# Optimization experiments

Hardware: AMD Instinct MI355X
Metric: run time of the kernel (lower is better)

## Reference

```python
import jax, jax.numpy as jnp
import numpy as np

FLOOR = 1e-06


def _ema(x, w):
    # x: [B, C, T], w: [C] clamped to [0, 1]
    w = jnp.clip(w, 0.0, 1.0)
    xt = jnp.moveaxis(x, 2, 0)  # [T, B, C]
    init = x[:, :, 0]           # [B, C]

    def step(acc, xi):
        acc = w * xi + (1.0 - w) * acc
        return acc, acc

    _, ys = jax.lax.scan(step, init, xt)  # ys: [T, B, C]
    return jnp.moveaxis(ys, 0, 2)         # [B, C, T]


def setup_inputs() -> dict:
    key = jax.random.key(0)
    k1, = jax.random.split(key, 1)
    B, C, T = 128, 64, 8000
    x = jax.random.uniform(k1, (B, C, T), dtype=jnp.float32)
    alpha = jnp.full((C,), 0.96, dtype=jnp.float32)
    delta = jnp.full((C,), 2.0, dtype=jnp.float32)
    root = jnp.full((C,), 2.0, dtype=jnp.float32)
    ema_weights = jnp.full((C,), 0.04, dtype=jnp.float32)
    return {"x": x, "alpha": alpha, "delta": delta, "root": root,
            "ema_weights": ema_weights}


def reference(x, alpha, delta, root, ema_weights):
    alpha = jnp.minimum(alpha, 1.0)          # [C]
    root = jnp.maximum(root, 1.0)            # [C]
    ema = _ema(x, ema_weights)               # [B, C, T]
    one_over_root = 1.0 / root
    a = alpha[None, :, None]
    d = delta[None, :, None]
    r = one_over_root[None, :, None]
    out = (x / (FLOOR + ema) ** a + d) ** r - d ** r
    return out
```

## Files before the change

kernel.cpp:

```cpp
#include <hip/hip_runtime.h>
#include <math.h>

#define T_LEN   8000
#define NT4     (T_LEN / 256)
#define TAILOFF (NT4 * 256)
#define FLOORV  1e-6f

__device__ __forceinline__ float pcen_pt(float xv, float em,
                                         float na, float d, float r, float dr)
{
    float u  = __builtin_amdgcn_exp2f(na * __builtin_amdgcn_logf(FLOORV + em));
    float b2 = fmaf(xv, u, d);
    return __builtin_amdgcn_exp2f(r * __builtin_amdgcn_logf(b2)) - dr;
}

__global__ __launch_bounds__(256, 8) void pcen_kernel(
    const float* __restrict__ x,
    const float* __restrict__ alpha,
    const float* __restrict__ delta,
    const float* __restrict__ root,
    const float* __restrict__ emaw,
    float* __restrict__ out,
    int C, int rows)
{
    const int wave = threadIdx.x >> 6;
    const int lane = threadIdx.x & 63;
    const int row  = blockIdx.x * 4 + wave;
    if (row >= rows) return;
    const int c = row % C;

    const float a  = fminf(alpha[c], 1.0f);
    const float d  = delta[c];
    const float rt = fmaxf(root[c], 1.0f);
    const float r  = 1.0f / rt;
    const float w  = fminf(fmaxf(emaw[c], 0.0f), 1.0f);
    const float q  = 1.0f - w;
    const float na = -a;
    const float dr = __builtin_amdgcn_exp2f(r * __builtin_amdgcn_logf(d));
    const float q2 = q * q, q4 = q2 * q2;

    const float*  xr  = x   + (size_t)row * T_LEN;
    float*        orw = out + (size_t)row * T_LEN;
    const float4* xv4 = (const float4*)xr;
    float4*       ov4 = (float4*)orw;

    float e = xr[0];

    float4 v = xv4[lane];
    for (int t = 0; t < NT4; ++t) {
        float4 cur = v;
        if (t + 1 < NT4) v = xv4[(t + 1) * 64 + lane];

        float A = w * cur.x;
        A = fmaf(q, A, w * cur.y);
        A = fmaf(q, A, w * cur.z);
        A = fmaf(q, A, w * cur.w);
        float D = q4;

        #pragma unroll
        for (int off = 1; off < 64; off <<= 1) {
            float Alo = __shfl_up(A, off);
            float Dlo = __shfl_up(D, off);
            if (lane >= off) { A = fmaf(D, Alo, A); D *= Dlo; }
        }

        float Aex = __shfl_up(A, 1);
        float Dex = __shfl_up(D, 1);
        float ein = (lane == 0) ? e : fmaf(Dex, e, Aex);

        float A63 = __shfl(A, 63);
        float D63 = __shfl(D, 63);
        float enext = fmaf(D63, e, A63);

        float e0 = fmaf(q, ein, w * cur.x);
        float e1 = fmaf(q, e0,  w * cur.y);
        float e2 = fmaf(q, e1,  w * cur.z);
        float e3 = fmaf(q, e2,  w * cur.w);
        float4 o;
        o.x = pcen_pt(cur.x, e0, na, d, r, dr);
        o.y = pcen_pt(cur.y, e1, na, d, r, dr);
        o.z = pcen_pt(cur.z, e2, na, d, r, dr);
        o.w = pcen_pt(cur.w, e3, na, d, r, dr);
        ov4[t * 64 + lane] = o;

        e = enext;
    }

    {
        float xt = xr[TAILOFF + lane];
        float A = w * xt;
        float D = q;
        #pragma unroll
        for (int off = 1; off < 64; off <<= 1) {
            float Alo = __shfl_up(A, off);
            float Dlo = __shfl_up(D, off);
            if (lane >= off) { A = fmaf(D, Alo, A); D *= Dlo; }
        }
        float em = fmaf(D, e, A);
        orw[TAILOFF + lane] = pcen_pt(xt, em, na, d, r, dr);
    }
}

extern "C" void kernel_launch(void* const* d_in, const int* in_sizes, int n_in,
                              void* d_out, int out_size, void* d_ws, size_t ws_size,
                              hipStream_t stream) {
    const float* x     = (const float*)d_in[0];
    const float* alpha = (const float*)d_in[1];
    const float* delta = (const float*)d_in[2];
    const float* root  = (const float*)d_in[3];
    const float* emaw  = (const float*)d_in[4];
    float* out = (float*)d_out;

    const int C    = in_sizes[1];
    const int rows = in_sizes[0] / T_LEN;

    const int blocks = (rows + 3) / 4;
    pcen_kernel<<<blocks, 256, 0, stream>>>(x, alpha, delta, root, emaw, out, C, rows);
}
```

Before: 451.6 us.

## Precompute decay powers for wave scan and deepen load prefetch to two tiles

The wave-level scan no longer carries and shuffles a decay factor D. Because the decay is a uniform power of q, the per-step multipliers q^(4*2^k), the per-lane prefix power and q^256 are computed once before the loop, which roughly halves the shuffles and multiplies per scan step. The tail scan gets the same treatment with powers of q. The x load is also prefetched two iterations ahead instead of one, costing an extra float4 of registers and a redundant reload of the last tile at the end.

```diff
diff --git a/kernel.cpp b/kernel.cpp
--- a/kernel.cpp
+++ b/kernel.cpp
@@ -37,7 +37,18 @@
     const float q  = 1.0f - w;
     const float na = -a;
     const float dr = __builtin_amdgcn_exp2f(r * __builtin_amdgcn_logf(d));
+
     const float q2 = q * q, q4 = q2 * q2;
+    const float c0 = q4, c1 = c0 * c0, c2 = c1 * c1,
+                c3 = c2 * c2, c4 = c3 * c3, c5 = c4 * c4;
+    const float q256 = c5 * c5;
+    float qpow = 1.0f;
+    qpow *= (lane & 1 ) ? c0 : 1.0f;
+    qpow *= (lane & 2 ) ? c1 : 1.0f;
+    qpow *= (lane & 4 ) ? c2 : 1.0f;
+    qpow *= (lane & 8 ) ? c3 : 1.0f;
+    qpow *= (lane & 16) ? c4 : 1.0f;
+    qpow *= (lane & 32) ? c5 : 1.0f;
 
     const float*  xr  = x   + (size_t)row * T_LEN;
     float*        orw = out + (size_t)row * T_LEN;
@@ -46,31 +57,33 @@
 
     float e = xr[0];
 
-    float4 v = xv4[lane];
+    float4 va = xv4[lane];
+    float4 vb = xv4[64 + lane];
+
     for (int t = 0; t < NT4; ++t) {
-        float4 cur = v;
-        if (t + 1 < NT4) v = xv4[(t + 1) * 64 + lane];
+        float4 cur = va;
+        va = vb;
+        const int pf = (t + 2 < NT4) ? (t + 2) : (NT4 - 1);
+        vb = xv4[pf * 64 + lane];
 
         float A = w * cur.x;
         A = fmaf(q, A, w * cur.y);
         A = fmaf(q, A, w * cur.z);
         A = fmaf(q, A, w * cur.w);
-        float D = q4;
 
-        #pragma unroll
-        for (int off = 1; off < 64; off <<= 1) {
-            float Alo = __shfl_up(A, off);
-            float Dlo = __shfl_up(D, off);
-            if (lane >= off) { A = fmaf(D, Alo, A); D *= Dlo; }
-        }
+        float s0 = __shfl_up(A, 1);  if (lane >= 1 ) A = fmaf(c0, s0, A);
+        float s1 = __shfl_up(A, 2);  if (lane >= 2 ) A = fmaf(c1, s1, A);
+        float s2 = __shfl_up(A, 4);  if (lane >= 4 ) A = fmaf(c2, s2, A);
+        float s3 = __shfl_up(A, 8);  if (lane >= 8 ) A = fmaf(c3, s3, A);
+        float s4 = __shfl_up(A, 16); if (lane >= 16) A = fmaf(c4, s4, A);
+        float s5 = __shfl_up(A, 32); if (lane >= 32) A = fmaf(c5, s5, A);
 
         float Aex = __shfl_up(A, 1);
-        float Dex = __shfl_up(D, 1);
-        float ein = (lane == 0) ? e : fmaf(Dex, e, Aex);
+        Aex = (lane == 0) ? 0.0f : Aex;
+        float ein = fmaf(qpow, e, Aex);
 
         float A63 = __shfl(A, 63);
-        float D63 = __shfl(D, 63);
-        float enext = fmaf(D63, e, A63);
+        float enext = fmaf(q256, e, A63);
 
         float e0 = fmaf(q, ein, w * cur.x);
         float e1 = fmaf(q, e0,  w * cur.y);
@@ -88,15 +101,23 @@
 
     {
         float xt = xr[TAILOFF + lane];
-        float A = w * xt;
-        float D = q;
-        #pragma unroll
-        for (int off = 1; off < 64; off <<= 1) {
-            float Alo = __shfl_up(A, off);
-            float Dlo = __shfl_up(D, off);
-            if (lane >= off) { A = fmaf(D, Alo, A); D *= Dlo; }
-        }
-        float em = fmaf(D, e, A);
+        float A  = w * xt;
+        const float d0 = q, d1 = d0 * d0, d2 = d1 * d1,
+                    d3 = d2 * d2, d4 = d3 * d3, d5 = d4 * d4;
+        float s0 = __shfl_up(A, 1);  if (lane >= 1 ) A = fmaf(d0, s0, A);
+        float s1 = __shfl_up(A, 2);  if (lane >= 2 ) A = fmaf(d1, s1, A);
+        float s2 = __shfl_up(A, 4);  if (lane >= 4 ) A = fmaf(d2, s2, A);
+        float s3 = __shfl_up(A, 8);  if (lane >= 8 ) A = fmaf(d3, s3, A);
+        float s4 = __shfl_up(A, 16); if (lane >= 16) A = fmaf(d4, s4, A);
+        float s5 = __shfl_up(A, 32); if (lane >= 32) A = fmaf(d5, s5, A);
+        float qpl = 1.0f;
+        qpl *= (lane & 1 ) ? d0 : 1.0f;
+        qpl *= (lane & 2 ) ? d1 : 1.0f;
+        qpl *= (lane & 4 ) ? d2 : 1.0f;
+        qpl *= (lane & 8 ) ? d3 : 1.0f;
+        qpl *= (lane & 16) ? d4 : 1.0f;
+        qpl *= (lane & 32) ? d5 : 1.0f;
+        float em = fmaf(q * qpl, e, A);
         orw[TAILOFF + lane] = pcen_pt(xt, em, na, d, r, dr);
     }
 }
```

Result: no change. 447.4 us (-0.9%).
